# Optimization experiments

Measured on AMD Instinct MI355X. Metric: run time of the kernel, lower is better.

The kernel has to match this reference:

```python
import jax, jax.numpy as jnp
import numpy as np

NEG_INF = -jnp.inf


def setup_inputs() -> dict:
    key = jax.random.key(0)
    ks = jax.random.split(key, 20)
    B, N, M = 8, 1024, 128
    F_OP, F_MA, F_E, OUT, HID = 64, 64, 16, 64, 128
    inp = {
        "x": jax.random.normal(ks[0], (B, N, F_OP), dtype=jnp.float32),
        "y": jax.random.normal(ks[1], (B, M, F_MA), dtype=jnp.float32),
        "z": jax.random.normal(ks[2], (B, N, M, F_E), dtype=jnp.float32),
        "op_adj_in": jax.random.randint(ks[3], (B, N, N), 0, 2, dtype=jnp.int32),
        "ma_adj_in": jax.random.randint(ks[4], (B, N, N), 0, 2, dtype=jnp.int32),
        "op_ma_adj": jax.random.randint(ks[5], (B, N, M), 0, 2, dtype=jnp.int32),
        # learned parameters
        "weight_op": jax.random.normal(ks[6], (F_OP, OUT), dtype=jnp.float32) * 0.1,
        "weight_ma": jax.random.normal(ks[7], (F_MA, OUT), dtype=jnp.float32) * 0.1,
        "weight_edge": jax.random.normal(ks[8], (F_E, OUT), dtype=jnp.float32) * 0.1,
        "attention_op": jax.random.normal(ks[9], (1, 2 * OUT), dtype=jnp.float32) * 0.1,
        "attention_ma": jax.random.normal(ks[10], (1, 3 * OUT), dtype=jnp.float32) * 0.1,
        "w1": jax.random.normal(ks[11], (2 * OUT, HID), dtype=jnp.float32) * 0.1,
        "b1": jnp.zeros((HID,), dtype=jnp.float32),
        "w2": jax.random.normal(ks[12], (HID, HID), dtype=jnp.float32) * 0.1,
        "b2": jnp.zeros((HID,), dtype=jnp.float32),
        "wo": jax.random.normal(ks[13], (HID, OUT), dtype=jnp.float32) * 0.1,
        "bo": jnp.zeros((OUT,), dtype=jnp.float32),
    }
    return inp


def reference(x, y, z, op_adj_in, ma_adj_in, op_ma_adj,
              weight_op, weight_ma, weight_edge, attention_op, attention_ma,
              w1, b1, w2, b2, wo, bo):
    OUT = weight_op.shape[1]
    h = jnp.einsum('bni,io->bno', x, weight_op)  # [B,N,OUT]
    # all_combinations[b,i,j] = cat(h[b,j], h[b,i]); dot with attention_op splits:
    a1 = attention_op[0, :OUT]
    a2 = attention_op[0, OUT:]
    e_op = (h @ a2)[:, :, None] + (h @ a1)[:, None, :]  # [B,N,N]
    e_op = jax.nn.leaky_relu(e_op, negative_slope=0.01)

    adj = (jnp.swapaxes(op_adj_in, 1, 2) + op_adj_in
           + jnp.swapaxes(ma_adj_in, 1, 2) + ma_adj_in)  # [B,N,N]
    row_mask = jnp.all(op_ma_adj == 0, axis=-1)  # [B,N] ops with no machine link
    adj = jnp.where(row_mask[:, :, None], 1, adj)
    att = jnp.where(adj > 0, e_op, NEG_INF)
    attention_in_op = jax.nn.softmax(att, axis=2)
    h_prime_op = jnp.einsum('bij,bjo->bio', attention_in_op, h)  # [B,N,OUT]

    h_ma = jnp.einsum('bmi,io->bmo', y, weight_ma)  # [B,M,OUT]
    h_edge = jnp.einsum('bnmi,io->bnmo', z, weight_edge)  # [B,N,M,OUT]
    # cat([h_op_i, h_ma_j, h_edge_ij]) @ attention_ma split into three dots
    am1 = attention_ma[0, :OUT]
    am2 = attention_ma[0, OUT:2 * OUT]
    am3 = attention_ma[0, 2 * OUT:]
    e_ma = (h @ am1)[:, :, None] + (h_ma @ am2)[:, None, :] + h_edge @ am3  # [B,N,M]
    e_ma = jax.nn.leaky_relu(e_ma, negative_slope=0.01)

    adj2 = jnp.where(row_mask[:, :, None], 1, op_ma_adj)
    att2 = jnp.where(adj2 > 0, e_ma, NEG_INF)
    attention_in_ma = jax.nn.softmax(att2, axis=2)  # [B,N,M]
    h_ma_edge = h_ma[:, None, :, :] + h_edge  # [B,N,M,OUT]
    h_prime_ma = jnp.einsum('bnm,bnmo->bno', attention_in_ma, h_ma_edge) + h

    h_prime = jnp.concatenate([h_prime_op, h_prime_ma], axis=-1)  # [B,N,2*OUT]
    embed = jax.nn.elu(h_prime @ w1 + b1)
    embed = jax.nn.elu(embed @ w2 + b2)
    embed = embed @ wo + bo
    embed = jnp.where(row_mask[:, :, None], 0.0, embed)
    return embed
```

## Files before the change

kernel.cpp:

```cpp
#include <hip/hip_runtime.h>
#include <math.h>

#define BB 8
#define NN 1024
#define MM 128
#define FOUT 64
#define HIDN 128

#define OFF_H       0
#define OFF_HMA     524288
#define OFF_HA1     589824
#define OFF_HA2     598016
#define OFF_HAM1    606208
#define OFF_HMAAM2  614400
#define OFF_RMASK   615424
#define OFF_WAM3    623616
#define OFF_HPRIME  623632
#define OFF_RDIR    1672208
#define OFF_OPMB    1934352
#define OFF_WT1HI   1967120
#define OFF_WT1LO   1975312
#define OFF_WT2HI   1983504
#define OFF_WT2LO   1991696
#define OFF_WTOHI   1999888
#define OFF_WTOLO   2003984
#define OFF_HTHI    2008080
#define OFF_HTLO    2270224
#define OFF_HMATHI  2532368
#define OFF_HMATLO  2565136
#define OFF_TRM     2597904

typedef __attribute__((ext_vector_type(8))) short bf16x8;
typedef __attribute__((ext_vector_type(8))) unsigned short u16x8;
typedef __attribute__((ext_vector_type(4))) float f32x4;

__device__ __forceinline__ void splitbf(float v, unsigned short& h, unsigned short& l) {
    unsigned u = __float_as_uint(v);
    unsigned hb = (u + 0x7FFFu + ((u >> 16) & 1u)) >> 16;
    float hf = __uint_as_float(hb << 16);
    float lf = v - hf;
    unsigned ul = __float_as_uint(lf);
    unsigned lb = (ul + 0x7FFFu + ((ul >> 16) & 1u)) >> 16;
    h = (unsigned short)hb; l = (unsigned short)lb;
}

__device__ __forceinline__ unsigned short tobf(float v) {
    unsigned u = __float_as_uint(v);
    return (unsigned short)((u + 0x7FFFu + ((u >> 16) & 1u)) >> 16);
}

__global__ __launch_bounds__(256) void k1_prep(
    const float* __restrict__ x, const float* __restrict__ y,
    const int* __restrict__ op_ma_adj,
    const int* __restrict__ op_adj, const int* __restrict__ ma_adj,
    const float* __restrict__ w_op, const float* __restrict__ w_ma,
    const float* __restrict__ w_edge,
    const float* __restrict__ att_op, const float* __restrict__ att_ma,
    const float* __restrict__ w1_g, const float* __restrict__ w2_g,
    const float* __restrict__ wo_g,
    float* __restrict__ h, float* __restrict__ h_ma,
    float* __restrict__ ha1, float* __restrict__ ha2, float* __restrict__ ham1,
    float* __restrict__ hmaam2, int* __restrict__ rmask, float* __restrict__ wam3,
    unsigned long long* __restrict__ rowdir, unsigned long long* __restrict__ opmb,
    unsigned short* __restrict__ trm,
    unsigned short* __restrict__ wt1hi, unsigned short* __restrict__ wt1lo,
    unsigned short* __restrict__ wt2hi, unsigned short* __restrict__ wt2lo,
    unsigned short* __restrict__ wtohi, unsigned short* __restrict__ wtolo,
    unsigned short* __restrict__ hthi, unsigned short* __restrict__ htlo,
    unsigned short* __restrict__ hmathi, unsigned short* __restrict__ hmatlo)
{
    __shared__ float wlds[64 * 64];
    __shared__ unsigned hstage[32 * 64];
    int bid = blockIdx.x;
    int t = threadIdx.x;
    int lane = t & 63;
    int wv = t >> 6;

    if (bid < 256) {
        int b = bid >> 5;
        int n0g = (bid & 31) * 32;
        for (int k = t; k < 4096; k += 256) wlds[k] = w_op[k];
        float a1c = att_op[lane], a2c = att_op[64 + lane], am1c = att_ma[lane];
        __syncthreads();
        #pragma unroll
        for (int p = 0; p < 8; ++p) {
            int row = b * NN + n0g + p * 4 + wv;
            float xv = x[(size_t)row * 64 + lane];
            float acc = 0.f;
            #pragma unroll
            for (int i = 0; i < 64; ++i) {
                float xi = __shfl(xv, i);
                acc += xi * wlds[i * 64 + lane];
            }
            h[(size_t)row * 64 + lane] = acc;
            unsigned short hs, ls;
            splitbf(acc, hs, ls);
            hstage[(p * 4 + wv) * 64 + lane] = (unsigned)hs | ((unsigned)ls << 16);
            float d1 = acc * a1c, d2 = acc * a2c, d3 = acc * am1c;
            #pragma unroll
            for (int m = 32; m; m >>= 1) {
                d1 += __shfl_xor(d1, m);
                d2 += __shfl_xor(d2, m);
                d3 += __shfl_xor(d3, m);
            }
            int v0 = op_ma_adj[(size_t)row * 128 + lane];
            int v1 = op_ma_adj[(size_t)row * 128 + 64 + lane];
            unsigned long long w0 = __ballot(v0 != 0);
            unsigned long long w1 = __ballot(v1 != 0);
            if (lane == 0) {
                ha1[row] = d1; ha2[row] = d2; ham1[row] = d3;
                opmb[row * 2] = w0; opmb[row * 2 + 1] = w1;
                rmask[row] = ((w0 | w1) == 0ULL) ? 1 : 0;
            }
        }
        __syncthreads();
        {
            int plane = t >> 7;
            int q = t & 127;
            int o = q >> 1;
            int hf = q & 1;
            int sh = plane * 16;
            unsigned short* dst = plane ? htlo : hthi;
            u16x8 pk0, pk1;
            #pragma unroll
            for (int k = 0; k < 8; ++k)
                pk0[k] = (unsigned short)((hstage[(hf * 16 + k) * 64 + o] >> sh) & 0xFFFFu);
            #pragma unroll
            for (int k = 0; k < 8; ++k)
                pk1[k] = (unsigned short)((hstage[(hf * 16 + 8 + k) * 64 + o] >> sh) & 0xFFFFu);
            size_t base = ((size_t)((bid >> 5) * 64 + o)) * 1024 + n0g + hf * 16;
            *(u16x8*)&dst[base] = pk0;
            *(u16x8*)&dst[base + 8] = pk1;
        }
    } else if (bid < 288) {
        int bb = (bid - 256) >> 2;
        int m0 = ((bid - 256) & 3) * 32;
        for (int k = t; k < 4096; k += 256) wlds[k] = w_ma[k];
        float am2c = att_ma[64 + lane];
        __syncthreads();
        #pragma unroll
        for (int p = 0; p < 8; ++p) {
            int row = bb * MM + m0 + p * 4 + wv;
            float yv = y[(size_t)row * 64 + lane];
            float acc = 0.f;
            #pragma unroll
            for (int i = 0; i < 64; ++i) {
                float yi = __shfl(yv, i);
                acc += yi * wlds[i * 64 + lane];
            }
            h_ma[(size_t)row * 64 + lane] = acc;
            unsigned short hs, ls;
            splitbf(acc, hs, ls);
            hstage[(p * 4 + wv) * 64 + lane] = (unsigned)hs | ((unsigned)ls << 16);
            float d = acc * am2c;
            #pragma unroll
            for (int m = 32; m; m >>= 1) d += __shfl_xor(d, m);
            if (lane == 0) hmaam2[row] = d;
        }
        __syncthreads();
        {
            int plane = t >> 7;
            int q = t & 127;
            int o = q >> 1;
            int hf = q & 1;
            int sh = plane * 16;
            unsigned short* dst = plane ? hmatlo : hmathi;
            u16x8 pk0, pk1;
            #pragma unroll
            for (int k = 0; k < 8; ++k)
                pk0[k] = (unsigned short)((hstage[(hf * 16 + k) * 64 + o] >> sh) & 0xFFFFu);
            #pragma unroll
            for (int k = 0; k < 8; ++k)
                pk1[k] = (unsigned short)((hstage[(hf * 16 + 8 + k) * 64 + o] >> sh) & 0xFFFFu);
            size_t base = ((size_t)(bb * 64 + o)) * 128 + m0 + hf * 16;
            *(u16x8*)&dst[base] = pk0;
            *(u16x8*)&dst[base + 8] = pk1;
        }
    } else if (bid == 288) {
        if (t < 16) {
            float s = 0.f;
            for (int o = 0; o < 64; ++o) s += w_edge[t * 64 + o] * att_ma[128 + o];
            wam3[t] = s;
        }
    } else if (bid < 2337) {
        unsigned char (*nib)[4][64] = (unsigned char(*)[4][64])wlds;
        int p = bid - 289;
        int b = p >> 8;
        int rg = p & 255;
        int rl = t >> 6;
        int row = rg * 4 + rl;
        const int4* oprow = (const int4*)(op_adj + ((size_t)(b * NN + row)) * NN);
        const int4* marow = (const int4*)(ma_adj + ((size_t)(b * NN + row)) * NN);
        #pragma unroll
        for (int p2 = 0; p2 < 4; ++p2) {
            int4 vo = oprow[p2 * 64 + lane];
            int4 vm = marow[p2 * 64 + lane];
            unsigned nb = ((vo.x | vm.x) ? 1u : 0u) | ((vo.y | vm.y) ? 2u : 0u)
                        | ((vo.z | vm.z) ? 4u : 0u) | ((vo.w | vm.w) ? 8u : 0u);
            nib[rl][p2][lane] = (unsigned char)nb;
        }
        __syncthreads();
        if (t < 64) {
            int arl = t >> 4, q = t & 15;
            const unsigned* nw = (const unsigned*)&nib[arl][q >> 2][(q & 3) * 16];
            unsigned long long w = 0;
            #pragma unroll
            for (int u = 0; u < 4; ++u) {
                unsigned v = nw[u];
                w |= (unsigned long long)(v & 0xFu)         << (16 * u);
                w |= (unsigned long long)((v >> 8) & 0xFu)  << (16 * u + 4);
                w |= (unsigned long long)((v >> 16) & 0xFu) << (16 * u + 8);
                w |= (unsigned long long)((v >> 24) & 0xFu) << (16 * u + 12);
            }
            int jrow = rg * 4 + arl;
            rowdir[((size_t)(b * NN + jrow)) * 16 + q] = w;
            #pragma unroll
            for (int s = 0; s < 4; ++s) {
                trm[((size_t)(b * 64 + q * 4 + s)) * 1024 + jrow] =
                    (unsigned short)((w >> (16 * s)) & 0xFFFFu);
            }
        }
    } else {
        float (*tls)[33] = (float(*)[33])wlds;
        int p = bid - 2337;
        const float* src; unsigned short *dhi, *dlo; int KD, CD, tI, tJ;
        if (p < 16)      { src = w1_g; dhi = wt1hi; dlo = wt1lo; KD = 128; CD = 128; tI = p >> 2; tJ = p & 3; }
        else if (p < 32) { src = w2_g; dhi = wt2hi; dlo = wt2lo; KD = 128; CD = 128; tI = (p-16) >> 2; tJ = (p-16) & 3; }
        else             { src = wo_g; dhi = wtohi; dlo = wtolo; KD = 128; CD = 64;  tI = (p-32) >> 1; tJ = (p-32) & 1; }
        int k0 = tI * 32, c0 = tJ * 32;
        #pragma unroll
        for (int it = 0; it < 4; ++it) {
            int r = (t >> 5) + it * 8;
            int c = t & 31;
            tls[r][c] = src[(size_t)(k0 + r) * CD + c0 + c];
        }
        __syncthreads();
        #pragma unroll
        for (int it = 0; it < 4; ++it) {
            int c = (t >> 5) + it * 8;
            int k = t & 31;
            unsigned short hs, ls;
            splitbf(tls[k][c], hs, ls);
            dhi[(size_t)(c0 + c) * KD + k0 + k] = hs;
            dlo[(size_t)(c0 + c) * KD + k0 + k] = ls;
        }
    }
}

__global__ __launch_bounds__(256) void k2_opatt(
    const unsigned long long* __restrict__ rowdir,
    const unsigned short* __restrict__ trm,
    const unsigned short* __restrict__ hthi,
    const unsigned short* __restrict__ htlo,
    const float* __restrict__ ha1, const float* __restrict__ ha2,
    const int* __restrict__ rmask, float* __restrict__ h_prime)
{
    __shared__ __align__(16) unsigned short Pl[16 * 1024];
    __shared__ float ha1s[1024];
    __shared__ unsigned long long dirw[16][16];
    __shared__ unsigned short trw[1024];
    __shared__ float rdeninv[16];
    int bid = blockIdx.x;
    int b = bid >> 6;
    int i0 = (bid & 63) << 4;
    int t = threadIdx.x;

    {
        int row = t >> 4, w = t & 15;
        dirw[row][w] = rowdir[((size_t)(b * NN + i0 + row)) * 16 + w];
    }
    {
        const unsigned* src = (const unsigned*)(trm + ((size_t)(b * 64 + (i0 >> 4))) * 1024);
        ((unsigned*)trw)[t] = src[t];
        ((unsigned*)trw)[t + 256] = src[t + 256];
    }
    ha1s[t] = ha1[b * NN + t];
    ha1s[t + 256] = ha1[b * NN + t + 256];
    ha1s[t + 512] = ha1[b * NN + t + 512];
    ha1s[t + 768] = ha1[b * NN + t + 768];
    __syncthreads();

    {
        int row = t >> 4, q = t & 15;
        int bn = b * NN + i0 + row;
        float ha2i = ha2[bn];
        unsigned rmf = rmask[bn] ? 1u : 0u;

        float mx = -INFINITY;
        #pragma unroll 8
        for (int jj = 0; jj < 64; ++jj) {
            int j = q + (jj << 4);
            float ev = ha2i + ha1s[j];
            ev = ev > 0.f ? ev : 0.01f * ev;
            unsigned bit = ((unsigned)(dirw[row][jj >> 2] >> (q + ((jj & 3) << 4))) & 1u)
                         | ((unsigned)(trw[j] >> row) & 1u) | rmf;
            if (bit) mx = fmaxf(mx, ev);
        }
        #pragma unroll
        for (int m = 1; m < 16; m <<= 1) mx = fmaxf(mx, __shfl_xor(mx, m));

        float s = 0.f;
        #pragma unroll 4
        for (int jj = 0; jj < 64; ++jj) {
            int j = q + (jj << 4);
            float ev = ha2i + ha1s[j];
            ev = ev > 0.f ? ev : 0.01f * ev;
            unsigned bit = ((unsigned)(dirw[row][jj >> 2] >> (q + ((jj & 3) << 4))) & 1u)
                         | ((unsigned)(trw[j] >> row) & 1u) | rmf;
            float u = bit ? __expf(ev - mx) : 0.f;
            s += u;
            unsigned short pb = tobf(u);
            unsigned byteoff = ((unsigned)(row * 2048 + j * 2)) ^ ((unsigned)((row & 7) << 4));
            *(unsigned short*)((char*)Pl + byteoff) = pb;
        }
        #pragma unroll
        for (int m = 1; m < 16; m <<= 1) s += __shfl_xor(s, m);
        if (q == 0) rdeninv[row] = 1.f / s;
    }
    __syncthreads();

    {
        int lane = t & 63, wvv = t >> 6;
        int arow = lane & 15, kg = lane >> 4;
        int col = wvv * 16 + arow;
        const unsigned short* bhp = hthi + ((size_t)(b * 64 + col)) * 1024;
        f32x4 acc = {0.f, 0.f, 0.f, 0.f};
        #pragma unroll 8
        for (int kst = 0; kst < 32; ++kst) {
            unsigned cc = ((unsigned)(kst * 4 + kg)) ^ ((unsigned)(arow & 7));
            bf16x8 pa = *(const bf16x8*)((char*)Pl + arow * 2048 + cc * 16);
            bf16x8 vh = *(const bf16x8*)&bhp[kst * 32 + kg * 8];
            acc = __builtin_amdgcn_mfma_f32_16x16x32_bf16(pa, vh, acc, 0, 0, 0);
        }
        size_t base = (size_t)(b * NN + i0);
        #pragma unroll
        for (int r = 0; r < 4; ++r) {
            int orow = kg * 4 + r;
            float v = acc[r] * rdeninv[orow];
            h_prime[(base + orow) * 128 + col] = v;
        }
    }
}

__global__ __launch_bounds__(256) void k3_maatt(
    const float* __restrict__ z, const unsigned long long* __restrict__ opmb,
    const float* __restrict__ h,
    const unsigned short* __restrict__ hmathi, const unsigned short* __restrict__ hmatlo,
    const float* __restrict__ ham1, const float* __restrict__ hmaam2,
    const int* __restrict__ rmask, const float* __restrict__ wam3,
    const float* __restrict__ w_edge, float* __restrict__ h_prime)
{
    __shared__ __align__(16) unsigned short U_lds[16 * 136];
    __shared__ float wedge_s[1024];
    __shared__ float wam3s[16];
    __shared__ float zsum_s[16][16];
    __shared__ float rdeninv[16];

    int bid = blockIdx.x;
    int b = bid >> 6;
    int n0 = (bid & 63) * 16;
    int t = threadIdx.x;
    int lane = t & 63;
    int wv = t >> 6;

    for (int k = t; k < 1024; k += 256) wedge_s[k] = w_edge[k];
    if (t < 16) wam3s[t] = wam3[t];
    __syncthreads();

    float hm0 = hmaam2[b * MM + lane];
    float hm1 = hmaam2[b * MM + 64 + lane];

    for (int pp = 0; pp < 4; ++pp) {
        int nl = pp * 4 + wv;
        int bn = b * NN + n0 + nl;
        const float4* zr = (const float4*)(z + (size_t)bn * MM * 16);
        float4 a0 = zr[lane * 4 + 0];
        float4 a1 = zr[lane * 4 + 1];
        float4 a2 = zr[lane * 4 + 2];
        float4 a3 = zr[lane * 4 + 3];
        float4 c0 = zr[(lane + 64) * 4 + 0];
        float4 c1 = zr[(lane + 64) * 4 + 1];
        float4 c2 = zr[(lane + 64) * 4 + 2];
        float4 c3 = zr[(lane + 64) * 4 + 3];

        float base = ham1[bn];
        float e0 = base + hm0;
        float e1 = base + hm1;
        e0 += a0.x*wam3s[0] + a0.y*wam3s[1] + a0.z*wam3s[2] + a0.w*wam3s[3]
            + a1.x*wam3s[4] + a1.y*wam3s[5] + a1.z*wam3s[6] + a1.w*wam3s[7]
            + a2.x*wam3s[8] + a2.y*wam3s[9] + a2.z*wam3s[10] + a2.w*wam3s[11]
            + a3.x*wam3s[12] + a3.y*wam3s[13] + a3.z*wam3s[14] + a3.w*wam3s[15];
        e1 += c0.x*wam3s[0] + c0.y*wam3s[1] + c0.z*wam3s[2] + c0.w*wam3s[3]
            + c1.x*wam3s[4] + c1.y*wam3s[5] + c1.z*wam3s[6] + c1.w*wam3s[7]
            + c2.x*wam3s[8] + c2.y*wam3s[9] + c2.z*wam3s[10] + c2.w*wam3s[11]
            + c3.x*wam3s[12] + c3.y*wam3s[13] + c3.z*wam3s[14] + c3.w*wam3s[15];
        e0 = e0 > 0.f ? e0 : 0.01f * e0;
        e1 = e1 > 0.f ? e1 : 0.01f * e1;
        unsigned long long bits0 = opmb[(size_t)bn * 2];
        unsigned long long bits1 = opmb[(size_t)bn * 2 + 1];
        int rm = rmask[bn];
        int v0 = rm | (int)((bits0 >> lane) & 1ULL);
        int v1 = rm | (int)((bits1 >> lane) & 1ULL);
        e0 = v0 ? e0 : -INFINITY;
        e1 = v1 ? e1 : -INFINITY;

        float mx = fmaxf(e0, e1);
        #pragma unroll
        for (int msk = 32; msk; msk >>= 1) mx = fmaxf(mx, __shfl_xor(mx, msk));
        float u0 = __expf(e0 - mx);
        float u1 = __expf(e1 - mx);
        float s = u0 + u1;
        #pragma unroll
        for (int msk = 32; msk; msk >>= 1) s += __shfl_xor(s, msk);

        U_lds[nl * 136 + lane] = tobf(u0);
        U_lds[nl * 136 + 64 + lane] = tobf(u1);
        if (lane == 0) rdeninv[nl] = 1.f / s;

        float zv[16];
        zv[0]=u0*a0.x+u1*c0.x;  zv[1]=u0*a0.y+u1*c0.y;
        zv[2]=u0*a0.z+u1*c0.z;  zv[3]=u0*a0.w+u1*c0.w;
        zv[4]=u0*a1.x+u1*c1.x;  zv[5]=u0*a1.y+u1*c1.y;
        zv[6]=u0*a1.z+u1*c1.z;  zv[7]=u0*a1.w+u1*c1.w;
        zv[8]=u0*a2.x+u1*c2.x;  zv[9]=u0*a2.y+u1*c2.y;
        zv[10]=u0*a2.z+u1*c2.z; zv[11]=u0*a2.w+u1*c2.w;
        zv[12]=u0*a3.x+u1*c3.x; zv[13]=u0*a3.y+u1*c3.y;
        zv[14]=u0*a3.z+u1*c3.z; zv[15]=u0*a3.w+u1*c3.w;
        #pragma unroll
        for (int s2 = 0; s2 < 8; ++s2) {
            float sel = (lane & 1) ? zv[s2] : zv[s2 + 8];
            float got = __shfl_xor(sel, 1);
            zv[s2] = ((lane & 1) ? zv[s2 + 8] : zv[s2]) + got;
        }
        #pragma unroll
        for (int s2 = 0; s2 < 4; ++s2) {
            float sel = (lane & 2) ? zv[s2] : zv[s2 + 4];
            float got = __shfl_xor(sel, 2);
            zv[s2] = ((lane & 2) ? zv[s2 + 4] : zv[s2]) + got;
        }
        #pragma unroll
        for (int s2 = 0; s2 < 2; ++s2) {
            float sel = (lane & 4) ? zv[s2] : zv[s2 + 2];
            float got = __shfl_xor(sel, 4);
            zv[s2] = ((lane & 4) ? zv[s2 + 2] : zv[s2]) + got;
        }
        {
            float sel = (lane & 8) ? zv[0] : zv[1];
            float got = __shfl_xor(sel, 8);
            zv[0] = ((lane & 8) ? zv[1] : zv[0]) + got;
        }
        zv[0] += __shfl_xor(zv[0], 16);
        zv[0] += __shfl_xor(zv[0], 32);
        if (lane < 16) {
            int comp = ((lane & 1) << 3) | ((lane & 2) << 1) | ((lane & 4) >> 1) | ((lane & 8) >> 3);
            zsum_s[nl][comp] = zv[0];
        }
    }
    __syncthreads();

    {
        int arow = lane & 15, kg = lane >> 4;
        int col = wv * 16 + arow;
        bf16x8 ua[4];
        #pragma unroll
        for (int ks = 0; ks < 4; ++ks)
            ua[ks] = *(const bf16x8*)&U_lds[arow * 136 + kg * 8 + ks * 32];
        const unsigned short* bhp = hmathi + ((size_t)(b * 64 + col)) * 128 + kg * 8;
        f32x4 acc = {0.f, 0.f, 0.f, 0.f};
        #pragma unroll
        for (int ks = 0; ks < 4; ++ks) {
            bf16x8 bh = *(const bf16x8*)&bhp[ks * 32];
            acc = __builtin_amdgcn_mfma_f32_16x16x32_bf16(ua[ks], bh, acc, 0, 0, 0);
        }
        #pragma unroll
        for (int r = 0; r < 4; ++r) {
            int row = kg * 4 + r;
            float he = 0.f;
            #pragma unroll
            for (int i = 0; i < 16; ++i) he += zsum_s[row][i] * wedge_s[i * 64 + col];
            int bn = b * NN + n0 + row;
            float val = (acc[r] + he) * rdeninv[row] + h[(size_t)bn * 64 + col];
            h_prime[(size_t)bn * 128 + 64 + col] = val;
        }
    }
}

__global__ __launch_bounds__(256) void k4_mlp(
    const float* __restrict__ hp, const int* __restrict__ rmask,
    const unsigned short* __restrict__ wt1hi, const unsigned short* __restrict__ wt1lo,
    const unsigned short* __restrict__ wt2hi, const unsigned short* __restrict__ wt2lo,
    const unsigned short* __restrict__ wtohi, const unsigned short* __restrict__ wtolo,
    const float* __restrict__ b1, const float* __restrict__ b2,
    const float* __restrict__ bo, float* __restrict__ out)
{
    __shared__ __align__(16) unsigned short Ahi0[16 * 136];
    __shared__ __align__(16) unsigned short Alo0[16 * 136];
    __shared__ __align__(16) unsigned short Ahi1[16 * 136];
    __shared__ __align__(16) unsigned short Alo1[16 * 136];
    __shared__ __align__(16) unsigned short Whi[64 * 128];
    __shared__ __align__(16) unsigned short Wlo[64 * 128];
    __shared__ int rml[16];
    int t = threadIdx.x;
    int lane = t & 63;
    int wv = t >> 6;
    int row0 = blockIdx.x * 16;
    int plane = t >> 7;
    int q = t & 127;

    {
        int r = t >> 4;
        int cg = (t & 15) * 8;
        const float* src = hp + (size_t)(row0 + r) * 128 + cg;
        float4 v0 = *(const float4*)src;
        float4 v1 = *(const float4*)(src + 4);
        float xs[8] = {v0.x, v0.y, v0.z, v0.w, v1.x, v1.y, v1.z, v1.w};
        u16x8 hv, lv;
        #pragma unroll
        for (int j = 0; j < 8; ++j) {
            unsigned short hs, ls;
            splitbf(xs[j], hs, ls);
            hv[j] = hs; lv[j] = ls;
        }
        *(u16x8*)&Ahi0[r * 136 + cg] = hv;
        *(u16x8*)&Alo0[r * 136 + cg] = lv;
        if (t < 16) rml[t] = rmask[row0 + t];
    }
    __syncthreads();

    int arow = lane & 15;
    int kg = lane >> 4;
    int aoff = arow * 136 + kg * 8;
    int lcol = wv * 16 + arow;

    {
        bf16x8 ah[4], al[4];
        #pragma unroll
        for (int ks = 0; ks < 4; ++ks) {
            ah[ks] = *(const bf16x8*)&Ahi0[aoff + ks * 32];
            al[ks] = *(const bf16x8*)&Alo0[aoff + ks * 32];
        }
        #pragma unroll
        for (int half = 0; half < 2; ++half) {
            __syncthreads();
            {
                const unsigned short* gsrc = plane ? wt1lo : wt1hi;
                char* dst = (char*)(plane ? Wlo : Whi);
                #pragma unroll
                for (int i = 0; i < 8; ++i) {
                    int L = q * 8 + i;
                    int col = L >> 4, kc = L & 15;
                    u16x8 v = *(const u16x8*)&gsrc[(size_t)(half * 64 + col) * 128 + kc * 8];
                    unsigned byteoff = ((unsigned)(col * 256 + kc * 16)) ^ ((unsigned)((col & 7) << 4));
                    *(u16x8*)(dst + byteoff) = v;
                }
            }
            __syncthreads();
            int col = half * 64 + lcol;
            f32x4 acc = {0.f, 0.f, 0.f, 0.f};
            #pragma unroll
            for (int ks = 0; ks < 4; ++ks) {
                unsigned wb = ((unsigned)(lcol * 256 + kg * 16 + ks * 64)) ^ ((unsigned)((arow & 7) << 4));
                bf16x8 bh = *(const bf16x8*)((char*)Whi + wb);
                bf16x8 bl = *(const bf16x8*)((char*)Wlo + wb);
                acc = __builtin_amdgcn_mfma_f32_16x16x32_bf16(ah[ks], bh, acc, 0, 0, 0);
                acc = __builtin_amdgcn_mfma_f32_16x16x32_bf16(al[ks], bh, acc, 0, 0, 0);
                acc = __builtin_amdgcn_mfma_f32_16x16x32_bf16(ah[ks], bl, acc, 0, 0, 0);
            }
            float bb = b1[col];
            #pragma unroll
            for (int r = 0; r < 4; ++r) {
                int row = kg * 4 + r;
                float v = acc[r] + bb;
                v = v > 0.f ? v : __expf(v) - 1.f;
                unsigned short hs, ls;
                splitbf(v, hs, ls);
                Ahi1[row * 136 + col] = hs;
                Alo1[row * 136 + col] = ls;
            }
        }
    }
    __syncthreads();

    {
        bf16x8 ah[4], al[4];
        #pragma unroll
        for (int ks = 0; ks < 4; ++ks) {
            ah[ks] = *(const bf16x8*)&Ahi1[aoff + ks * 32];
            al[ks] = *(const bf16x8*)&Alo1[aoff + ks * 32];
        }
        #pragma unroll
        for (int half = 0; half < 2; ++half) {
            __syncthreads();
            {
                const unsigned short* gsrc = plane ? wt2lo : wt2hi;
                char* dst = (char*)(plane ? Wlo : Whi);
                #pragma unroll
                for (int i = 0; i < 8; ++i) {
                    int L = q * 8 + i;
                    int col = L >> 4, kc = L & 15;
                    u16x8 v = *(const u16x8*)&gsrc[(size_t)(half * 64 + col) * 128 + kc * 8];
                    unsigned byteoff = ((unsigned)(col * 256 + kc * 16)) ^ ((unsigned)((col & 7) << 4));
                    *(u16x8*)(dst + byteoff) = v;
                }
            }
            __syncthreads();
            int col = half * 64 + lcol;
            f32x4 acc = {0.f, 0.f, 0.f, 0.f};
            #pragma unroll
            for (int ks = 0; ks < 4; ++ks) {
                unsigned wb = ((unsigned)(lcol * 256 + kg * 16 + ks * 64)) ^ ((unsigned)((arow & 7) << 4));
                bf16x8 bh = *(const bf16x8*)((char*)Whi + wb);
                bf16x8 bl = *(const bf16x8*)((char*)Wlo + wb);
                acc = __builtin_amdgcn_mfma_f32_16x16x32_bf16(ah[ks], bh, acc, 0, 0, 0);
                acc = __builtin_amdgcn_mfma_f32_16x16x32_bf16(al[ks], bh, acc, 0, 0, 0);
                acc = __builtin_amdgcn_mfma_f32_16x16x32_bf16(ah[ks], bl, acc, 0, 0, 0);
            }
            float bb = b2[col];
            #pragma unroll
            for (int r = 0; r < 4; ++r) {
                int row = kg * 4 + r;
                float v = acc[r] + bb;
                v = v > 0.f ? v : __expf(v) - 1.f;
                unsigned short hs, ls;
                splitbf(v, hs, ls);
                Ahi0[row * 136 + col] = hs;
                Alo0[row * 136 + col] = ls;
            }
        }
    }
    __syncthreads();

    {
        bf16x8 ah[4], al[4];
        #pragma unroll
        for (int ks = 0; ks < 4; ++ks) {
            ah[ks] = *(const bf16x8*)&Ahi0[aoff + ks * 32];
            al[ks] = *(const bf16x8*)&Alo0[aoff + ks * 32];
        }
        __syncthreads();
        {
            const unsigned short* gsrc = plane ? wtolo : wtohi;
            char* dst = (char*)(plane ? Wlo : Whi);
            #pragma unroll
            for (int i = 0; i < 8; ++i) {
                int L = q * 8 + i;
                int col = L >> 4, kc = L & 15;
                u16x8 v = *(const u16x8*)&gsrc[(size_t)col * 128 + kc * 8];
                unsigned byteoff = ((unsigned)(col * 256 + kc * 16)) ^ ((unsigned)((col & 7) << 4));
                *(u16x8*)(dst + byteoff) = v;
            }
        }
        __syncthreads();
        int col = lcol;
        f32x4 acc = {0.f, 0.f, 0.f, 0.f};
        #pragma unroll
        for (int ks = 0; ks < 4; ++ks) {
            unsigned wb = ((unsigned)(lcol * 256 + kg * 16 + ks * 64)) ^ ((unsigned)((arow & 7) << 4));
            bf16x8 bh = *(const bf16x8*)((char*)Whi + wb);
            bf16x8 bl = *(const bf16x8*)((char*)Wlo + wb);
            acc = __builtin_amdgcn_mfma_f32_16x16x32_bf16(ah[ks], bh, acc, 0, 0, 0);
            acc = __builtin_amdgcn_mfma_f32_16x16x32_bf16(al[ks], bh, acc, 0, 0, 0);
            acc = __builtin_amdgcn_mfma_f32_16x16x32_bf16(ah[ks], bl, acc, 0, 0, 0);
        }
        float bb = bo[col];
        #pragma unroll
        for (int r = 0; r < 4; ++r) {
            int row = kg * 4 + r;
            float v = acc[r] + bb;
            out[(size_t)(row0 + row) * 64 + col] = rml[row] ? 0.f : v;
        }
    }
}

extern "C" void kernel_launch(void* const* d_in, const int* in_sizes, int n_in,
                              void* d_out, int out_size, void* d_ws, size_t ws_size,
                              hipStream_t stream) {
    const float* x      = (const float*)d_in[0];
    const float* y      = (const float*)d_in[1];
    const float* z      = (const float*)d_in[2];
    const int*   op_adj = (const int*)d_in[3];
    const int*   ma_adj = (const int*)d_in[4];
    const int*   opma   = (const int*)d_in[5];
    const float* w_op   = (const float*)d_in[6];
    const float* w_ma   = (const float*)d_in[7];
    const float* w_edge = (const float*)d_in[8];
    const float* att_op = (const float*)d_in[9];
    const float* att_ma = (const float*)d_in[10];
    const float* w1     = (const float*)d_in[11];
    const float* b1     = (const float*)d_in[12];
    const float* w2     = (const float*)d_in[13];
    const float* b2     = (const float*)d_in[14];
    const float* wo     = (const float*)d_in[15];
    const float* bo     = (const float*)d_in[16];
    float* out = (float*)d_out;

    float* ws = (float*)d_ws;
    float* h       = ws + OFF_H;
    float* h_ma    = ws + OFF_HMA;
    float* ha1     = ws + OFF_HA1;
    float* ha2     = ws + OFF_HA2;
    float* ham1    = ws + OFF_HAM1;
    float* hmaam2  = ws + OFF_HMAAM2;
    int*   rmask   = (int*)(ws + OFF_RMASK);
    float* wam3    = ws + OFF_WAM3;
    float* h_prime = ws + OFF_HPRIME;
    unsigned long long* rowdir = (unsigned long long*)(ws + OFF_RDIR);
    unsigned long long* opmb = (unsigned long long*)(ws + OFF_OPMB);
    unsigned short* trm   = (unsigned short*)(ws + OFF_TRM);
    unsigned short* wt1hi = (unsigned short*)(ws + OFF_WT1HI);
    unsigned short* wt1lo = (unsigned short*)(ws + OFF_WT1LO);
    unsigned short* wt2hi = (unsigned short*)(ws + OFF_WT2HI);
    unsigned short* wt2lo = (unsigned short*)(ws + OFF_WT2LO);
    unsigned short* wtohi = (unsigned short*)(ws + OFF_WTOHI);
    unsigned short* wtolo = (unsigned short*)(ws + OFF_WTOLO);
    unsigned short* hthi  = (unsigned short*)(ws + OFF_HTHI);
    unsigned short* htlo  = (unsigned short*)(ws + OFF_HTLO);
    unsigned short* hmathi = (unsigned short*)(ws + OFF_HMATHI);
    unsigned short* hmatlo = (unsigned short*)(ws + OFF_HMATLO);

    k1_prep<<<256 + 32 + 1 + 2048 + 40, 256, 0, stream>>>(
        x, y, opma, op_adj, ma_adj, w_op, w_ma, w_edge, att_op, att_ma,
        w1, w2, wo,
        h, h_ma, ha1, ha2, ham1, hmaam2, rmask, wam3, rowdir, opmb, trm,
        wt1hi, wt1lo, wt2hi, wt2lo, wtohi, wtolo, hthi, htlo, hmathi, hmatlo);

    k2_opatt<<<512, 256, 0, stream>>>(
        rowdir, trm, hthi, htlo, ha1, ha2, rmask, h_prime);

    k3_maatt<<<512, 256, 0, stream>>>(
        z, opmb, h, hmathi, hmatlo, ham1, hmaam2, rmask, wam3, w_edge, h_prime);

    k4_mlp<<<512, 256, 0, stream>>>(
        h_prime, rmask, wt1hi, wt1lo, wt2hi, wt2lo, wtohi, wtolo,
        b1, b2, bo, out);
}
```

Baseline: 84.21 us.

## Shrink ma-attention blocks to four rows and simplify op-attention max

The ma-attention kernel now handles 4 op rows per block instead of 16, launching four times as many blocks so more of the z stream is in flight at once. Each wave processes one row with no inner loop. The cost is that the 16x16 MFMA now computes padded rows, and only a quarter of the lanes write output. The op-attention max pass uses monotonicity of leaky-relu to take the max over ha1 and apply the activation once, cutting ALU work. Unused lo-plane arguments are dropped, and a k1 index uses a named batch variable.

```diff
diff --git a/kernel.cpp b/kernel.cpp
--- a/kernel.cpp
+++ b/kernel.cpp
@@ -128,7 +128,7 @@
             #pragma unroll
             for (int k = 0; k < 8; ++k)
                 pk1[k] = (unsigned short)((hstage[(hf * 16 + 8 + k) * 64 + o] >> sh) & 0xFFFFu);
-            size_t base = ((size_t)((bid >> 5) * 64 + o)) * 1024 + n0g + hf * 16;
+            size_t base = ((size_t)(b * 64 + o)) * 1024 + n0g + hf * 16;
             *(u16x8*)&dst[base] = pk0;
             *(u16x8*)&dst[base + 8] = pk1;
         }
@@ -251,7 +251,6 @@
     const unsigned long long* __restrict__ rowdir,
     const unsigned short* __restrict__ trm,
     const unsigned short* __restrict__ hthi,
-    const unsigned short* __restrict__ htlo,
     const float* __restrict__ ha1, const float* __restrict__ ha2,
     const int* __restrict__ rmask, float* __restrict__ h_prime)
 {
@@ -286,18 +285,18 @@
         float ha2i = ha2[bn];
         unsigned rmf = rmask[bn] ? 1u : 0u;
 
-        float mx = -INFINITY;
+        float mh = -INFINITY;
         #pragma unroll 8
         for (int jj = 0; jj < 64; ++jj) {
             int j = q + (jj << 4);
-            float ev = ha2i + ha1s[j];
-            ev = ev > 0.f ? ev : 0.01f * ev;
             unsigned bit = ((unsigned)(dirw[row][jj >> 2] >> (q + ((jj & 3) << 4))) & 1u)
                          | ((unsigned)(trw[j] >> row) & 1u) | rmf;
-            if (bit) mx = fmaxf(mx, ev);
-        }
-        #pragma unroll
-        for (int m = 1; m < 16; m <<= 1) mx = fmaxf(mx, __shfl_xor(mx, m));
+            if (bit) mh = fmaxf(mh, ha1s[j]);
+        }
+        #pragma unroll
+        for (int m = 1; m < 16; m <<= 1) mh = fmaxf(mh, __shfl_xor(mh, m));
+        float mx = ha2i + mh;
+        mx = mx > 0.f ? mx : 0.01f * mx;
 
         float s = 0.f;
         #pragma unroll 4
@@ -345,20 +344,20 @@
 __global__ __launch_bounds__(256) void k3_maatt(
     const float* __restrict__ z, const unsigned long long* __restrict__ opmb,
     const float* __restrict__ h,
-    const unsigned short* __restrict__ hmathi, const unsigned short* __restrict__ hmatlo,
+    const unsigned short* __restrict__ hmathi,
     const float* __restrict__ ham1, const float* __restrict__ hmaam2,
     const int* __restrict__ rmask, const float* __restrict__ wam3,
     const float* __restrict__ w_edge, float* __restrict__ h_prime)
 {
-    __shared__ __align__(16) unsigned short U_lds[16 * 136];
+    __shared__ __align__(16) unsigned short U_lds[4 * 136];
     __shared__ float wedge_s[1024];
     __shared__ float wam3s[16];
-    __shared__ float zsum_s[16][16];
-    __shared__ float rdeninv[16];
+    __shared__ float zsum_s[4][16];
+    __shared__ float rdeninv[4];
 
     int bid = blockIdx.x;
-    int b = bid >> 6;
-    int n0 = (bid & 63) * 16;
+    int b = bid >> 8;
+    int n0 = (bid & 255) * 4;
     int t = threadIdx.x;
     int lane = t & 63;
     int wv = t >> 6;
@@ -367,12 +366,8 @@
     if (t < 16) wam3s[t] = wam3[t];
     __syncthreads();
 
-    float hm0 = hmaam2[b * MM + lane];
-    float hm1 = hmaam2[b * MM + 64 + lane];
-
-    for (int pp = 0; pp < 4; ++pp) {
-        int nl = pp * 4 + wv;
-        int bn = b * NN + n0 + nl;
+    {
+        int bn = b * NN + n0 + wv;
         const float4* zr = (const float4*)(z + (size_t)bn * MM * 16);
         float4 a0 = zr[lane * 4 + 0];
         float4 a1 = zr[lane * 4 + 1];
@@ -383,6 +378,8 @@
         float4 c2 = zr[(lane + 64) * 4 + 2];
         float4 c3 = zr[(lane + 64) * 4 + 3];
 
+        float hm0 = hmaam2[b * MM + lane];
+        float hm1 = hmaam2[b * MM + 64 + lane];
         float base = ham1[bn];
         float e0 = base + hm0;
         float e1 = base + hm1;
@@ -413,9 +410,9 @@
         #pragma unroll
         for (int msk = 32; msk; msk >>= 1) s += __shfl_xor(s, msk);
 
-        U_lds[nl * 136 + lane] = tobf(u0);
-        U_lds[nl * 136 + 64 + lane] = tobf(u1);
-        if (lane == 0) rdeninv[nl] = 1.f / s;
+        U_lds[wv * 136 + lane] = tobf(u0);
+        U_lds[wv * 136 + 64 + lane] = tobf(u1);
+        if (lane == 0) rdeninv[wv] = 1.f / s;
 
         float zv[16];
         zv[0]=u0*a0.x+u1*c0.x;  zv[1]=u0*a0.y+u1*c0.y;
@@ -453,7 +450,7 @@
         zv[0] += __shfl_xor(zv[0], 32);
         if (lane < 16) {
             int comp = ((lane & 1) << 3) | ((lane & 2) << 1) | ((lane & 4) >> 1) | ((lane & 8) >> 3);
-            zsum_s[nl][comp] = zv[0];
+            zsum_s[wv][comp] = zv[0];
         }
     }
     __syncthreads();
@@ -464,7 +461,7 @@
         bf16x8 ua[4];
         #pragma unroll
         for (int ks = 0; ks < 4; ++ks)
-            ua[ks] = *(const bf16x8*)&U_lds[arow * 136 + kg * 8 + ks * 32];
+            ua[ks] = *(const bf16x8*)&U_lds[(arow & 3) * 136 + kg * 8 + ks * 32];
         const unsigned short* bhp = hmathi + ((size_t)(b * 64 + col)) * 128 + kg * 8;
         f32x4 acc = {0.f, 0.f, 0.f, 0.f};
         #pragma unroll
@@ -472,15 +469,16 @@
             bf16x8 bh = *(const bf16x8*)&bhp[ks * 32];
             acc = __builtin_amdgcn_mfma_f32_16x16x32_bf16(ua[ks], bh, acc, 0, 0, 0);
         }
-        #pragma unroll
-        for (int r = 0; r < 4; ++r) {
-            int row = kg * 4 + r;
-            float he = 0.f;
-            #pragma unroll
-            for (int i = 0; i < 16; ++i) he += zsum_s[row][i] * wedge_s[i * 64 + col];
-            int bn = b * NN + n0 + row;
-            float val = (acc[r] + he) * rdeninv[row] + h[(size_t)bn * 64 + col];
-            h_prime[(size_t)bn * 128 + 64 + col] = val;
+        if (kg == 0) {
+            #pragma unroll
+            for (int r = 0; r < 4; ++r) {
+                float he = 0.f;
+                #pragma unroll
+                for (int i = 0; i < 16; ++i) he += zsum_s[r][i] * wedge_s[i * 64 + col];
+                int bn = b * NN + n0 + r;
+                float val = (acc[r] + he) * rdeninv[r] + h[(size_t)bn * 64 + col];
+                h_prime[(size_t)bn * 128 + 64 + col] = val;
+            }
         }
     }
 }
@@ -725,10 +723,10 @@
         wt1hi, wt1lo, wt2hi, wt2lo, wtohi, wtolo, hthi, htlo, hmathi, hmatlo);
 
     k2_opatt<<<512, 256, 0, stream>>>(
-        rowdir, trm, hthi, htlo, ha1, ha2, rmask, h_prime);
-
-    k3_maatt<<<512, 256, 0, stream>>>(
-        z, opmb, h, hmathi, hmatlo, ham1, hmaam2, rmask, wam3, w_edge, h_prime);
+        rowdir, trm, hthi, ha1, ha2, rmask, h_prime);
+
+    k3_maatt<<<2048, 256, 0, stream>>>(
+        z, opmb, h, hmathi, ham1, hmaam2, rmask, wam3, w_edge, h_prime);
 
     k4_mlp<<<512, 256, 0, stream>>>(
         h_prime, rmask, wt1hi, wt1lo, wt2hi, wt2lo, wtohi, wtolo,
```

Result: no change. 85.41 us (+1.4%).
